# Kernel tuning notes

Hardware: AMD Instinct MI355X
Metric: run time of the kernel (lower is better)

## Reference

```python
import jax, jax.numpy as jnp
import numpy as np
from jax import lax

T_SIZE = 8        # frames
S_SIZE = 14       # spatial grid side
N_HEAD = 16
D_MODEL = 1024
L = S_SIZE * S_SIZE          # 196 patch tokens per frame
N_BATCH = 8


def _layernorm(x, g, b):
    # torch LayerNorm subclass computes in fp32 then casts back
    x32 = x.astype(jnp.float32)
    m = x32.mean(-1, keepdims=True)
    v = x32.var(-1, keepdims=True)
    return ((x32 - m) * lax.rsqrt(v + 1e-5) * g + b).astype(x.dtype)


def _mha(x, wqkv, bqkv, wo, bo, bias):
    # x: [S, B, C] seq-first like torch MHA; bias: [n_head, S, S] or None
    S, B, C = x.shape
    hd = C // N_HEAD
    qkv = x @ wqkv.T + bqkv
    q, k, v = jnp.split(qkv, 3, axis=-1)
    def h(t):
        return t.reshape(S, B, N_HEAD, hd).transpose(1, 2, 0, 3)  # [B,H,S,hd]
    q = h(q) * (1.0 / np.sqrt(hd))
    k, v = h(k), h(v)
    scores = jnp.einsum('bhqd,bhkd->bhqk', q, k)
    if bias is not None:
        scores = scores + bias[None]  # broadcast over batch (torch repeats; same math)
    a = jax.nn.softmax(scores, axis=-1)
    o = jnp.einsum('bhqk,bhkd->bhqd', a, v).transpose(2, 0, 1, 3).reshape(S, B, C)
    return o @ wo.T + bo


def _rel_idx():
    t = jnp.arange(T_SIZE)
    idx_t = t[:, None] - t[None, :] + T_SIZE - 1          # [T,T]
    c = jnp.arange(L)
    qi, qj = c // S_SIZE, c % S_SIZE
    i_off = qi[:, None] - qi[None, :] + S_SIZE - 1
    j_off = qj[:, None] - qj[None, :] + S_SIZE - 1
    idx_s = i_off * (2 * S_SIZE - 1) + j_off              # [L,L]
    return idx_t, idx_s


def reference(x, pos_w, pos_b, ln_t_g, ln_t_b, rpb_t, wqkv_t, bqkv_t, wo_t, bo_t,
              ln1_g, ln1_b, rpb_s, wqkv_s, bqkv_s, wo_s, bo_s,
              ln2_g, ln2_b, fc_w, fc_b, proj_w, proj_b):
    T, S, H, C = T_SIZE, S_SIZE, N_HEAD, D_MODEL
    LT = L * T
    N = x.shape[1]
    idx_t, idx_s = _rel_idx()

    # depthwise 3D conv positional embedding on patch tokens (token order is (h w t))
    v = x[1:].reshape(S, S, T, N, C).transpose(3, 4, 2, 0, 1)  # [N,C,T,H,W]
    conv = lax.conv_general_dilated(
        v, pos_w, (1, 1, 1), [(1, 1), (1, 1), (1, 1)],
        dimension_numbers=('NCDHW', 'OIDHW', 'NCDHW'),
        feature_group_count=C) + pos_b[None, :, None, None, None]
    tmp = (v + conv).reshape(N, C, T, L).transpose(3, 2, 0, 1).reshape(LT, N, C)
    x = jnp.concatenate([x[:1], tmp], 0)

    # temporal attention: '(l t) n c -> t (n l) c'
    xt = x[1:].reshape(L, T, N, C).transpose(1, 2, 0, 3).reshape(T, N * L, C)
    bias_t = rpb_t[idx_t].transpose(2, 0, 1)  # [H,T,T]
    rt = _mha(_layernorm(xt, ln_t_g, ln_t_b), wqkv_t, bqkv_t, wo_t, bo_t, bias_t)
    rt = rt.reshape(T, N, L, C).transpose(2, 0, 1, 3).reshape(LT, N, C)
    xt_full = x[1:] + rt

    # spatial attention with replicated cls token: 'l (t n) c' batching
    cls = jnp.tile(x[:1], (1, T, 1))                      # [1, T*N, C], t-major
    xs = jnp.concatenate([cls, xt_full.reshape(L, T * N, C)], 0)  # [L+1, T*N, C]
    bias_s = jnp.zeros((H, L + 1, L + 1), x.dtype).at[:, 1:, 1:].set(
        rpb_s[idx_s].transpose(2, 0, 1))
    rs = _mha(_layernorm(xs, ln1_g, ln1_b), wqkv_s, bqkv_s, wo_s, bo_s, bias_s)
    cls_out = rs[0].reshape(T, N, C).mean(0, keepdims=True)       # mean over frames
    spa = rs[1:].reshape(LT, N, C)                                # 'l (t n) -> (l t) n'
    x = x + jnp.concatenate([cls_out, spa], 0)

    # MLP with QuickGELU
    h = _layernorm(x, ln2_g, ln2_b) @ fc_w.T + fc_b
    h = h * jax.nn.sigmoid(1.702 * h)
    return x + (h @ proj_w.T + proj_b)


def setup_inputs() -> dict:
    key = jax.random.key(0)
    ks = jax.random.split(key, 12)
    C = D_MODEL
    f32 = jnp.float32
    def w(k, shape, s=0.02):
        return jax.random.normal(k, shape, f32) * s
    return {
        'x': jax.random.normal(ks[0], (1 + L * T_SIZE, N_BATCH, C), f32),
        'pos_w': w(ks[1], (C, 1, 3, 3, 3)),
        'pos_b': jnp.zeros((C,), f32),
        'ln_t_g': jnp.ones((C,), f32), 'ln_t_b': jnp.zeros((C,), f32),
        'rpb_t': w(ks[2], (2 * T_SIZE - 1, N_HEAD)),
        'wqkv_t': w(ks[3], (3 * C, C)), 'bqkv_t': jnp.zeros((3 * C,), f32),
        'wo_t': w(ks[4], (C, C)), 'bo_t': jnp.zeros((C,), f32),
        'ln1_g': jnp.ones((C,), f32), 'ln1_b': jnp.zeros((C,), f32),
        'rpb_s': w(ks[5], ((2 * S_SIZE - 1) ** 2, N_HEAD)),
        'wqkv_s': w(ks[6], (3 * C, C)), 'bqkv_s': jnp.zeros((3 * C,), f32),
        'wo_s': w(ks[7], (C, C)), 'bo_s': jnp.zeros((C,), f32),
        'ln2_g': jnp.ones((C,), f32), 'ln2_b': jnp.zeros((C,), f32),
        'fc_w': w(ks[8], (4 * C, C)), 'fc_b': jnp.zeros((4 * C,), f32),
        'proj_w': w(ks[9], (C, 4 * C)), 'proj_b': jnp.zeros((C,), f32),
    }
```

## Files before the change

### kernel.cpp

```cpp
#include <hip/hip_runtime.h>
#include <stdint.h>

typedef unsigned short u16;
typedef __attribute__((ext_vector_type(8))) __bf16 bf16x8;
typedef __attribute__((ext_vector_type(4))) float f32x4;

__device__ __forceinline__ float bf2f(u16 u) {
    return __uint_as_float(((unsigned int)u) << 16);
}
__device__ __forceinline__ u16 f2bf(float f) {
    unsigned int u = __float_as_uint(f);
    u += 0x7fffu + ((u >> 16) & 1u);
    return (u16)(u >> 16);
}

__device__ __forceinline__ void gl16(const u16* g, u16* l) {
    __builtin_amdgcn_global_load_lds(
        (const __attribute__((address_space(1))) unsigned int*)(uintptr_t)g,
        (__attribute__((address_space(3))) unsigned int*)(uintptr_t)l,
        16, 0, 0);
}

__global__ __launch_bounds__(256) void cvt_bf16(const float4* __restrict__ in,
                                                ushort4* __restrict__ out, int n4) {
    int tid = blockIdx.x * 256 + threadIdx.x;
    if (tid < n4) {
        float4 v = in[tid];
        ushort4 o;
        o.x = f2bf(v.x); o.y = f2bf(v.y); o.z = f2bf(v.z); o.w = f2bf(v.w);
        out[tid] = o;
    }
}

__global__ __launch_bounds__(256) void cvt_wt(const float* __restrict__ pw,
                                              float* __restrict__ wt) {
    int tid = blockIdx.x * 256 + threadIdx.x;
    if (tid < 27648) {
        int tap = tid >> 10, c = tid & 1023;
        wt[tid] = pw[c * 27 + tap];
    }
}

__global__ __launch_bounds__(256) void posembed(const float4* __restrict__ x4,
                                                const float4* __restrict__ wt4,
                                                const float4* __restrict__ pb4,
                                                float4* __restrict__ out4) {
    int tid = blockIdx.x * 256 + threadIdx.x;
    float4 xv = x4[tid];
    int rf = tid >> 11;
    if (rf == 0) { out4[tid] = xv; return; }
    int c4 = tid & 255;
    int n = (tid >> 8) & 7;
    int r = rf - 1;
    int t = r & 7, l = r >> 3;
    int i = l / 14, j = l - i * 14;
    float4 pbv = pb4[c4];
    float a0 = xv.x + pbv.x, a1 = xv.y + pbv.y, a2 = xv.z + pbv.z, a3 = xv.w + pbv.w;
#pragma unroll
    for (int dt = 0; dt < 3; dt++) {
        int tt = t + dt - 1;
        if (tt < 0 || tt > 7) continue;
#pragma unroll
        for (int di = 0; di < 3; di++) {
            int ii = i + di - 1;
            if (ii < 0 || ii > 13) continue;
#pragma unroll
            for (int dj = 0; dj < 3; dj++) {
                int jj = j + dj - 1;
                if (jj < 0 || jj > 13) continue;
                float4 w4 = wt4[(dt * 9 + di * 3 + dj) * 256 + c4];
                float4 v = x4[(size_t)(1 + ((ii * 14 + jj) << 3) + tt) * 2048 + (n << 8) + c4];
                a0 += w4.x * v.x; a1 += w4.y * v.y; a2 += w4.z * v.z; a3 += w4.w * v.w;
            }
        }
    }
    out4[tid] = (float4){a0, a1, a2, a3};
}

__global__ __launch_bounds__(256) void ln_kernel(const float* __restrict__ resid,
                                                 const u16* __restrict__ Radd,
                                                 const float* __restrict__ g,
                                                 const float* __restrict__ bb,
                                                 u16* __restrict__ out, int mode) {
    int ro = blockIdx.x;
    int tid = threadIdx.x;
    int src, n;
    long long rarow = -1;
    if (mode == 0) {
        int t = ro / 1568, b2 = ro - t * 1568;
        n = b2 / 196;
        int l = b2 - n * 196;
        src = 1 + l * 8 + t;
    } else if (mode == 1) {
        int s = ro >> 6, u = ro & 63;
        int t = u >> 3;
        n = u & 7;
        if (s == 0) src = 0;
        else { src = 1 + (s - 1) * 8 + t; rarow = (long long)(t * 1568 + n * 196 + (s - 1)); }
    } else {
        src = ro >> 3;
        n = ro & 7;
    }
    const float* xp = resid + ((size_t)src * 8 + n) * 1024 + tid * 4;
    float4 xv = *(const float4*)xp;
    float x0 = xv.x, x1 = xv.y, x2 = xv.z, x3 = xv.w;
    if (rarow >= 0) {
        const u16* rp = Radd + rarow * 1024 + tid * 4;
        x0 += bf2f(rp[0]); x1 += bf2f(rp[1]); x2 += bf2f(rp[2]); x3 += bf2f(rp[3]);
    }
    float s1 = x0 + x1 + x2 + x3;
    float s2 = x0 * x0 + x1 * x1 + x2 * x2 + x3 * x3;
#pragma unroll
    for (int off = 32; off > 0; off >>= 1) {
        s1 += __shfl_down(s1, off);
        s2 += __shfl_down(s2, off);
    }
    __shared__ float red[8];
    int lane = tid & 63, w = tid >> 6;
    if (lane == 0) { red[w] = s1; red[4 + w] = s2; }
    __syncthreads();
    float S1 = red[0] + red[1] + red[2] + red[3];
    float S2 = red[4] + red[5] + red[6] + red[7];
    float mean = S1 * (1.f / 1024.f);
    float var = S2 * (1.f / 1024.f) - mean * mean;
    float rstd = rsqrtf(var + 1e-5f);
    int c = tid * 4;
    u16* op = out + (size_t)ro * 1024 + c;
    op[0] = f2bf((x0 - mean) * rstd * g[c + 0] + bb[c + 0]);
    op[1] = f2bf((x1 - mean) * rstd * g[c + 1] + bb[c + 1]);
    op[2] = f2bf((x2 - mean) * rstd * g[c + 2] + bb[c + 2]);
    op[3] = f2bf((x3 - mean) * rstd * g[c + 3] + bb[c + 3]);
}

__global__ __launch_bounds__(256) void gemm_bf16(const u16* __restrict__ A,
                                                 const u16* __restrict__ W,
                                                 const float* __restrict__ bias,
                                                 u16* __restrict__ Co,
                                                 int M, int N, int K, int gelu,
                                                 int nx) {
    __shared__ u16 As[2][128 * 32];
    __shared__ u16 Bs[2][128 * 32];
    int tid = threadIdx.x;
    int T = gridDim.x;
    int bid = blockIdx.x;
    int w_ = (bid & 7) * (T >> 3) + (bid >> 3);
    int n0 = (w_ % nx) * 128;
    int m0 = (w_ / nx) * 128;
    int lane = tid & 63, wid = tid >> 6;
    int wm = (wid >> 1) * 64, wn = (wid & 1) * 64;
    int lm = lane & 15, q = lane >> 4;

    f32x4 acc[4][4];
#pragma unroll
    for (int i = 0; i < 4; i++)
#pragma unroll
        for (int j = 0; j < 4; j++) acc[i][j] = (f32x4){0.f, 0.f, 0.f, 0.f};

    int r0 = wid * 32 + (lane >> 2);
    int colb = (lane & 3) * 8;
    int mA0 = m0 + r0;          if (mA0 > M - 1) mA0 = M - 1;
    int mA1 = m0 + r0 + 16;     if (mA1 > M - 1) mA1 = M - 1;
    const u16* gA0 = A + (size_t)mA0 * K + colb;
    const u16* gA1 = A + (size_t)mA1 * K + colb;
    const u16* gB0 = W + (size_t)(n0 + r0) * K + colb;
    const u16* gB1 = W + (size_t)(n0 + r0 + 16) * K + colb;
    int wo = wid * 1024;

    auto loadt = [&](int b) {
        gl16(gA0, &As[b][wo]); gl16(gA1, &As[b][wo + 512]);
        gl16(gB0, &Bs[b][wo]); gl16(gB1, &Bs[b][wo + 512]);
        gA0 += 32; gA1 += 32; gB0 += 32; gB1 += 32;
    };
    auto comput = [&](int b) {
        bf16x8 af[4], bfr[4];
#pragma unroll
        for (int i = 0; i < 4; i++) af[i] = *(const bf16x8*)&As[b][(wm + i * 16 + lm) * 32 + q * 8];
#pragma unroll
        for (int j = 0; j < 4; j++) bfr[j] = *(const bf16x8*)&Bs[b][(wn + j * 16 + lm) * 32 + q * 8];
#pragma unroll
        for (int i = 0; i < 4; i++)
#pragma unroll
            for (int j = 0; j < 4; j++)
                acc[i][j] = __builtin_amdgcn_mfma_f32_16x16x32_bf16(af[i], bfr[j], acc[i][j], 0, 0, 0);
    };

    int Tt = K >> 5;
    loadt(0);
    __syncthreads();
    loadt(1); comput(0); __syncthreads();
    for (int t = 2; t + 1 < Tt; t += 2) {
        loadt(0); comput(1); __syncthreads();
        loadt(1); comput(0); __syncthreads();
    }
    comput(1);

#pragma unroll
    for (int i = 0; i < 4; i++) {
        int row_b = m0 + wm + i * 16 + q * 4;
#pragma unroll
        for (int j = 0; j < 4; j++) {
            int col = n0 + wn + j * 16 + lm;
            float bv = bias[col];
#pragma unroll
            for (int r = 0; r < 4; r++) {
                int row = row_b + r;
                if (row < M) {
                    float v = acc[i][j][r] + bv;
                    if (gelu) v = v / (1.f + __expf(-1.702f * v));
                    Co[(size_t)row * N + col] = f2bf(v);
                }
            }
        }
    }
}

__global__ __launch_bounds__(512) void gemm256(const u16* __restrict__ A,
                                               const u16* __restrict__ W,
                                               const float* __restrict__ bias,
                                               u16* __restrict__ Co,
                                               float* __restrict__ Fout,
                                               int M, int N, int K, int gelu,
                                               int nnt) {
    __shared__ __align__(16) u16 sA[2][16384];
    __shared__ __align__(16) u16 sB[2][16384];
    int tid = threadIdx.x;
    int wid = tid >> 6, lane = tid & 63;
    int wr = wid >> 2, wc = wid & 3;
    int lm = lane & 15, q = lane >> 4;

    int nwg = gridDim.x, orig = blockIdx.x;
    int qq = nwg >> 3, rr = nwg & 7, xcd = orig & 7, blk = orig >> 3;
    int wg = (xcd < rr ? xcd * (qq + 1) : rr * (qq + 1) + (xcd - rr) * qq) + blk;
    int n0 = (wg % nnt) * 256, m0 = (wg / nnt) * 256;

    int NT = K >> 6, NTm1 = NT - 1;

    int rl = wid * 8 + (lane >> 3);
    int cl = ((lane & 7) ^ (rl & 7)) * 8;
    const u16* pA[4];
    const u16* pB[4];
#pragma unroll
    for (int h2 = 0; h2 < 4; h2++) {
        int ra = m0 + h2 * 64 + rl; if (ra > M - 1) ra = M - 1;
        int rb = n0 + h2 * 64 + rl; if (rb > N - 1) rb = N - 1;
        pA[h2] = A + (size_t)ra * K + cl;
        pB[h2] = W + (size_t)rb * K + cl;
    }
    int ldst = wid * 512;

    f32x4 acc[8][4];
#pragma unroll
    for (int i = 0; i < 8; i++)
#pragma unroll
        for (int j = 0; j < 4; j++) acc[i][j] = (f32x4){0.f, 0.f, 0.f, 0.f};

    bf16x8 af[4][2];
    bf16x8 bfv[4][2];

#define STG(P, D, b, h, kt) do { \
        int _k = (kt); if (_k > NTm1) _k = NTm1; \
        gl16(P[(h) * 2] + (size_t)_k * 64, &D[b][(h) * 8192 + ldst]); \
        gl16(P[(h) * 2 + 1] + (size_t)_k * 64, &D[b][(h) * 8192 + 4096 + ldst]); \
    } while (0)
#define LDA_(b, ih) do { \
        _Pragma("unroll") for (int iq = 0; iq < 4; iq++) \
        _Pragma("unroll") for (int kk = 0; kk < 2; kk++) \
            af[iq][kk] = *(const bf16x8*)&sA[b][((ih) * 128 + wr * 64 + iq * 16 + lm) * 64 + \
                                                (((q + kk * 4) ^ (lm & 7)) * 8)]; \
    } while (0)
#define LDB_(b, jh) do { \
        _Pragma("unroll") for (int jq = 0; jq < 2; jq++) \
        _Pragma("unroll") for (int kk = 0; kk < 2; kk++) \
            bfv[(jh) * 2 + jq][kk] = *(const bf16x8*)&sB[b][((jh) * 128 + wc * 32 + jq * 16 + lm) * 64 + \
                                                            (((q + kk * 4) ^ (lm & 7)) * 8)]; \
    } while (0)
#define MMA_(ih, jh) do { \
        __builtin_amdgcn_s_setprio(1); \
        _Pragma("unroll") for (int iq = 0; iq < 4; iq++) \
        _Pragma("unroll") for (int jq = 0; jq < 2; jq++) \
        _Pragma("unroll") for (int kk = 0; kk < 2; kk++) \
            acc[(ih) * 4 + iq][(jh) * 2 + jq] = __builtin_amdgcn_mfma_f32_16x16x32_bf16( \
                af[iq][kk], bfv[(jh) * 2 + jq][kk], acc[(ih) * 4 + iq][(jh) * 2 + jq], 0, 0, 0); \
        __builtin_amdgcn_s_setprio(0); \
    } while (0)
#define BAR asm volatile("s_barrier" ::: "memory")
#define VM6 asm volatile("s_waitcnt vmcnt(6)" ::: "memory")

    STG(pA, sA, 0, 0, 0);
    STG(pA, sA, 0, 1, 0);
    STG(pB, sB, 0, 0, 0);
    STG(pB, sB, 0, 1, 0);
    STG(pA, sA, 1, 0, 1);
    STG(pB, sB, 1, 1, 1);
    STG(pA, sA, 1, 1, 1);
    VM6;
    BAR;

    int S = NT >> 1;
    for (int s = 0; s < S; s++) {
        int t = s * 2;
        LDA_(0, 0); LDB_(0, 0);
        STG(pB, sB, 1, 0, t + 1);
        BAR; MMA_(0, 0); BAR;
        LDB_(0, 1);
        STG(pA, sA, 0, 0, t + 2);
        BAR; MMA_(0, 1); BAR;
        LDA_(0, 1);
        STG(pB, sB, 0, 1, t + 2);
        BAR; MMA_(1, 1); BAR;
        STG(pA, sA, 0, 1, t + 2);
        VM6;
        BAR; MMA_(1, 0); BAR;
        LDA_(1, 0); LDB_(1, 0);
        STG(pB, sB, 0, 0, t + 2);
        BAR; MMA_(0, 0); BAR;
        LDB_(1, 1);
        STG(pA, sA, 1, 0, t + 3);
        BAR; MMA_(0, 1); BAR;
        LDA_(1, 1);
        STG(pB, sB, 1, 1, t + 3);
        BAR; MMA_(1, 1); BAR;
        STG(pA, sA, 1, 1, t + 3);
        VM6;
        BAR; MMA_(1, 0); BAR;
    }
    asm volatile("s_waitcnt vmcnt(0)" ::: "memory");

#pragma unroll
    for (int ih = 0; ih < 2; ih++)
#pragma unroll
        for (int iq = 0; iq < 4; iq++) {
            int row_b = m0 + ih * 128 + wr * 64 + iq * 16 + q * 4;
#pragma unroll
            for (int jh = 0; jh < 2; jh++)
#pragma unroll
                for (int jq = 0; jq < 2; jq++) {
                    int col = n0 + jh * 128 + wc * 32 + jq * 16 + lm;
                    float bv = bias[col];
#pragma unroll
                    for (int r = 0; r < 4; r++) {
                        int row = row_b + r;
                        if (row < M) {
                            float v = acc[ih * 4 + iq][jh * 2 + jq][r] + bv;
                            if (gelu) v = v / (1.f + __expf(-1.702f * v));
                            if (Fout) {
                                size_t o = (size_t)row * N + col;
                                Fout[o] = Fout[o] + v;
                            } else {
                                Co[(size_t)row * N + col] = f2bf(v);
                            }
                        }
                    }
                }
        }
#undef STG
#undef LDA_
#undef LDB_
#undef MMA_
#undef BAR
#undef VM6
}

__global__ __launch_bounds__(64) void attn_t(const u16* __restrict__ qkv,
                                             const float* __restrict__ rpb,
                                             u16* __restrict__ out) {
    int blk = blockIdx.x;
    int b = blk % 1568, h = blk / 1568;
    int d = threadIdx.x;
    __shared__ float qs[8][65], ks[8][65], vs[8][65];
    __shared__ float ps[8][9];
#pragma unroll
    for (int t = 0; t < 8; t++) {
        size_t row = (size_t)(t * 1568 + b) * 3072 + h * 64 + d;
        qs[t][d] = bf2f(qkv[row]) * 0.125f;
        ks[t][d] = bf2f(qkv[row + 1024]);
        vs[t][d] = bf2f(qkv[row + 2048]);
    }
    __syncthreads();
    int tq = d >> 3, tk = d & 7;
    float s = rpb[(tq - tk + 7) * 16 + h];
#pragma unroll
    for (int dd = 0; dd < 64; dd++) s += qs[tq][dd] * ks[tk][dd];
    float mx = s;
    mx = fmaxf(mx, __shfl_xor(mx, 1));
    mx = fmaxf(mx, __shfl_xor(mx, 2));
    mx = fmaxf(mx, __shfl_xor(mx, 4));
    float p = __expf(s - mx);
    float su = p;
    su += __shfl_xor(su, 1);
    su += __shfl_xor(su, 2);
    su += __shfl_xor(su, 4);
    ps[tq][tk] = p / su;
    __syncthreads();
#pragma unroll
    for (int t2 = 0; t2 < 8; t2++) {
        float o = 0.f;
#pragma unroll
        for (int k2 = 0; k2 < 8; k2++) o += ps[t2][k2] * vs[k2][d];
        out[(size_t)(t2 * 1568 + b) * 1024 + h * 64 + d] = f2bf(o);
    }
}

#define KLS 72
#define PVS 232
__global__ __launch_bounds__(256) void attn_s(const u16* __restrict__ qkv,
                                              const float* __restrict__ rpb,
                                              u16* __restrict__ out) {
    __shared__ u16 Kl[208 * KLS];
    __shared__ u16 Vt[64 * PVS];
    __shared__ u16 Pl[4][16 * PVS];
    __shared__ float rpb_l[736];
    int blk = blockIdx.x;
    int u = blk & 63, h = blk >> 6;
    int tid = threadIdx.x;
    int w = tid >> 6, lane = tid & 63;
    int lm = lane & 15, quad = lane >> 4;

    for (int idx = tid; idx < 197 * 8; idx += 256) {
        int s = idx >> 3, c8 = idx & 7;
        const u16* gp = qkv + (size_t)(s * 64 + u) * 3072 + h * 64 + c8 * 8;
        uint4 kv = *(const uint4*)(gp + 1024);
        uint4 vv = *(const uint4*)(gp + 2048);
        *(uint4*)&Kl[s * KLS + c8 * 8] = kv;
        const u16* vp = (const u16*)&vv;
#pragma unroll
        for (int j = 0; j < 8; j++) Vt[(c8 * 8 + j) * PVS + s] = vp[j];
    }
    for (int i = tid; i < 11 * KLS; i += 256) Kl[197 * KLS + i] = 0;
    for (int i = tid; i < 64 * 35; i += 256) {
        int dd = i / 35, c = 197 + (i - dd * 35);
        Vt[dd * PVS + c] = 0;
    }
    {
        for (int i = lane; i < 256; i += 64) {
            int r = i >> 4, c = 208 + (i & 15);
            Pl[w][r * PVS + c] = 0;
        }
    }
    for (int i = tid; i < 729; i += 256) rpb_l[i] = rpb[i * 16 + h];
    __syncthreads();

    for (int it = 0; it < 4; it++) {
        int qt = it * 4 + w;
        bool act = qt < 13;
        f32x4 sc[13];
        float rs[4];
        if (act) {
            int qrow = qt * 16 + lm;
            int srq = qrow > 196 ? 196 : qrow;
            const u16* qp = qkv + (size_t)(srq * 64 + u) * 3072 + h * 64 + quad * 8;
            bf16x8 aq0 = *(const bf16x8*)qp;
            bf16x8 aq1 = *(const bf16x8*)(qp + 32);
            for (int kt = 0; kt < 13; kt++) {
                bf16x8 bk0 = *(const bf16x8*)&Kl[(kt * 16 + lm) * KLS + quad * 8];
                bf16x8 bk1 = *(const bf16x8*)&Kl[(kt * 16 + lm) * KLS + 32 + quad * 8];
                f32x4 s = __builtin_amdgcn_mfma_f32_16x16x32_bf16(aq0, bk0, (f32x4){0.f, 0.f, 0.f, 0.f}, 0, 0, 0);
                sc[kt] = __builtin_amdgcn_mfma_f32_16x16x32_bf16(aq1, bk1, s, 0, 0, 0);
            }
            int tk = lm;
#pragma unroll
            for (int r = 0; r < 4; r++) {
                int qr = qt * 16 + quad * 4 + r;
                int qcl = qr > 196 ? 196 : qr;
                int lq = qcl - 1;
                int qi = lq / 14, qj = lq - qi * 14;
                for (int kt = 0; kt < 13; kt++) {
                    int tkk = kt * 16 + tk;
                    float v;
                    if (tkk >= 197) v = -1e30f;
                    else {
                        v = sc[kt][r] * 0.125f;
                        if (qr >= 1 && tkk >= 1) {
                            int lk = tkk - 1;
                            int ki = lk / 14, kj = lk - ki * 14;
                            v += rpb_l[(qi - ki + 13) * 27 + (qj - kj + 13)];
                        }
                    }
                    sc[kt][r] = v;
                }
                float mx = -3e38f;
                for (int kt = 0; kt < 13; kt++) mx = fmaxf(mx, sc[kt][r]);
                mx = fmaxf(mx, __shfl_xor(mx, 1));
                mx = fmaxf(mx, __shfl_xor(mx, 2));
                mx = fmaxf(mx, __shfl_xor(mx, 4));
                mx = fmaxf(mx, __shfl_xor(mx, 8));
                float sm = 0.f;
                for (int kt = 0; kt < 13; kt++) {
                    float p = __expf(sc[kt][r] - mx);
                    sc[kt][r] = p;
                    sm += p;
                }
                sm += __shfl_xor(sm, 1);
                sm += __shfl_xor(sm, 2);
                sm += __shfl_xor(sm, 4);
                sm += __shfl_xor(sm, 8);
                rs[r] = sm;
                for (int kt = 0; kt < 13; kt++)
                    Pl[w][(quad * 4 + r) * PVS + kt * 16 + tk] = f2bf(sc[kt][r]);
            }
        }
        __syncthreads();
        if (act) {
            bf16x8 pa[7];
#pragma unroll
            for (int kc = 0; kc < 7; kc++)
                pa[kc] = *(const bf16x8*)&Pl[w][lm * PVS + kc * 32 + quad * 8];
#pragma unroll
            for (int ct = 0; ct < 4; ct++) {
                f32x4 o = (f32x4){0.f, 0.f, 0.f, 0.f};
#pragma unroll
                for (int kc = 0; kc < 7; kc++) {
                    bf16x8 vb = *(const bf16x8*)&Vt[(ct * 16 + lm) * PVS + kc * 32 + quad * 8];
                    o = __builtin_amdgcn_mfma_f32_16x16x32_bf16(pa[kc], vb, o, 0, 0, 0);
                }
#pragma unroll
                for (int r = 0; r < 4; r++) {
                    int qr = qt * 16 + quad * 4 + r;
                    if (qr < 197)
                        out[(size_t)(qr * 64 + u) * 1024 + h * 64 + ct * 16 + lm] =
                            f2bf(o[r] / rs[r]);
                }
            }
        }
        __syncthreads();
    }
}

__global__ __launch_bounds__(256) void add_cls(const u16* __restrict__ R, float4* __restrict__ resid4) {
    int tid = blockIdx.x * 256 + threadIdx.x;
    int c4 = tid & 255, n = tid >> 8;
    float s0 = 0.f, s1 = 0.f, s2 = 0.f, s3 = 0.f;
#pragma unroll
    for (int t = 0; t < 8; t++) {
        ushort4 rv = *(const ushort4*)&R[(size_t)(t * 8 + n) * 1024 + c4 * 4];
        s0 += bf2f(rv.x); s1 += bf2f(rv.y); s2 += bf2f(rv.z); s3 += bf2f(rv.w);
    }
    float4 v = resid4[tid];
    v.x += s0 * 0.125f; v.y += s1 * 0.125f; v.z += s2 * 0.125f; v.w += s3 * 0.125f;
    resid4[tid] = v;
}

__global__ __launch_bounds__(256) void add_spa(const u16* __restrict__ R, float4* __restrict__ resid4) {
    int tid = blockIdx.x * 256 + threadIdx.x;
    int c4 = tid & 255;
    int n = (tid >> 8) & 7;
    int r = tid >> 11;
    int t = r & 7, l = r >> 3;
    int srow = (l + 1) * 64 + t * 8 + n;
    ushort4 rv = *(const ushort4*)&R[(size_t)srow * 1024 + c4 * 4];
    float4 v = resid4[tid + 2048];
    v.x += bf2f(rv.x); v.y += bf2f(rv.y); v.z += bf2f(rv.z); v.w += bf2f(rv.w);
    resid4[tid + 2048] = v;
}

extern "C" void kernel_launch(void* const* d_in, const int* in_sizes, int n_in,
                              void* d_out, int out_size, void* d_ws, size_t ws_size,
                              hipStream_t stream) {
    const float* x      = (const float*)d_in[0];
    const float* pos_w  = (const float*)d_in[1];
    const float* pos_b  = (const float*)d_in[2];
    const float* ln_t_g = (const float*)d_in[3];
    const float* ln_t_b = (const float*)d_in[4];
    const float* rpb_t  = (const float*)d_in[5];
    const float* wqkv_t = (const float*)d_in[6];
    const float* bqkv_t = (const float*)d_in[7];
    const float* wo_t   = (const float*)d_in[8];
    const float* bo_t   = (const float*)d_in[9];
    const float* ln1_g  = (const float*)d_in[10];
    const float* ln1_b  = (const float*)d_in[11];
    const float* rpb_s  = (const float*)d_in[12];
    const float* wqkv_s = (const float*)d_in[13];
    const float* bqkv_s = (const float*)d_in[14];
    const float* wo_s   = (const float*)d_in[15];
    const float* bo_s   = (const float*)d_in[16];
    const float* ln2_g  = (const float*)d_in[17];
    const float* ln2_b  = (const float*)d_in[18];
    const float* fc_w   = (const float*)d_in[19];
    const float* fc_b   = (const float*)d_in[20];
    const float* proj_w = (const float*)d_in[21];
    const float* proj_b = (const float*)d_in[22];
    float* resid = (float*)d_out;

    u16* Wq_t  = (u16*)d_ws;
    u16* Wo_t  = Wq_t + 3145728;
    u16* Wq_s  = Wo_t + 1048576;
    u16* Wo_s  = Wq_s + 3145728;
    u16* Wfc   = Wo_s + 1048576;
    u16* Wpj   = Wfc  + 4194304;
    u16* Albuf = Wpj  + 4194304;
    u16* QKV   = Albuf + 12910592;
    u16* Obuf  = QKV   + 38731776;
    u16* Rbuf  = Obuf  + 12910592;
    u16* Hbuf  = QKV;
    float* wt  = (float*)QKV;

    cvt_bf16<<<3072, 256, 0, stream>>>((const float4*)wqkv_t, (ushort4*)Wq_t, 786432);
    cvt_bf16<<<1024, 256, 0, stream>>>((const float4*)wo_t,   (ushort4*)Wo_t, 262144);
    cvt_bf16<<<3072, 256, 0, stream>>>((const float4*)wqkv_s, (ushort4*)Wq_s, 786432);
    cvt_bf16<<<1024, 256, 0, stream>>>((const float4*)wo_s,   (ushort4*)Wo_s, 262144);
    cvt_bf16<<<4096, 256, 0, stream>>>((const float4*)fc_w,   (ushort4*)Wfc,  1048576);
    cvt_bf16<<<4096, 256, 0, stream>>>((const float4*)proj_w, (ushort4*)Wpj,  1048576);
    cvt_wt<<<108, 256, 0, stream>>>(pos_w, wt);

    posembed<<<12552, 256, 0, stream>>>((const float4*)x, (const float4*)wt,
                                        (const float4*)pos_b, (float4*)resid);

    ln_kernel<<<12544, 256, 0, stream>>>(resid, nullptr, ln_t_g, ln_t_b, Albuf, 0);
    gemm_bf16<<<2352, 256, 0, stream>>>(Albuf, Wq_t, bqkv_t, QKV, 12544, 3072, 1024, 0, 24);
    attn_t<<<25088, 64, 0, stream>>>(QKV, rpb_t, Obuf);
    gemm_bf16<<<784, 256, 0, stream>>>(Obuf, Wo_t, bo_t, Rbuf, 12544, 1024, 1024, 0, 8);

    ln_kernel<<<12608, 256, 0, stream>>>(resid, Rbuf, ln1_g, ln1_b, Albuf, 1);
    gemm_bf16<<<2376, 256, 0, stream>>>(Albuf, Wq_s, bqkv_s, QKV, 12608, 3072, 1024, 0, 24);
    attn_s<<<1024, 256, 0, stream>>>(QKV, rpb_s, Obuf);
    gemm_bf16<<<792, 256, 0, stream>>>(Obuf, Wo_s, bo_s, Rbuf, 12608, 1024, 1024, 0, 8);
    add_cls<<<8, 256, 0, stream>>>(Rbuf, (float4*)resid);
    add_spa<<<12544, 256, 0, stream>>>(Rbuf, (float4*)resid);

    ln_kernel<<<12552, 256, 0, stream>>>(resid, nullptr, ln2_g, ln2_b, Albuf, 2);
    gemm_bf16<<<3168, 256, 0, stream>>>(Albuf, Wfc, fc_b, Hbuf, 12552, 4096, 1024, 1, 32);
    gemm256<<<200, 512, 0, stream>>>(Hbuf, Wpj, proj_b, nullptr, resid,
                                     12552, 1024, 4096, 0, 4);
}
```

Baseline: 1.152 ms.

## Fuse spatial residual add into out-proj GEMM, merge weight casts, vectorize loads

The separate weight-conversion launches become one multi-segment kernel. The spatial-attention output projection now adds its result straight into the fp32 residual for patch rows and writes bf16 only for the cls rows, which removes the add_spa kernel and its bf16 round trip. LayerNorm gamma/beta and the temporal-attention QKV loads are vectorized, and the shared-memory padding changes. The fused epilogue does scattered fp32 read-modify-write stores, and it skips the bf16 rounding of R for spatial rows, which slightly changes numerics.

```diff
diff --git a/kernel.cpp b/kernel.cpp
--- a/kernel.cpp
+++ b/kernel.cpp
@@ -21,15 +21,25 @@
         16, 0, 0);
 }
 
-__global__ __launch_bounds__(256) void cvt_bf16(const float4* __restrict__ in,
-                                                ushort4* __restrict__ out, int n4) {
-    int tid = blockIdx.x * 256 + threadIdx.x;
-    if (tid < n4) {
-        float4 v = in[tid];
-        ushort4 o;
-        o.x = f2bf(v.x); o.y = f2bf(v.y); o.z = f2bf(v.z); o.w = f2bf(v.w);
-        out[tid] = o;
-    }
+__global__ __launch_bounds__(256) void cvt_all(const float4* __restrict__ a0, ushort4* __restrict__ o0,
+                                               const float4* __restrict__ a1, ushort4* __restrict__ o1,
+                                               const float4* __restrict__ a2, ushort4* __restrict__ o2,
+                                               const float4* __restrict__ a3, ushort4* __restrict__ o3,
+                                               const float4* __restrict__ a4, ushort4* __restrict__ o4,
+                                               const float4* __restrict__ a5, ushort4* __restrict__ o5) {
+    int b = blockIdx.x;
+    const float4* src; ushort4* dst; int base;
+    if      (b < 3072)  { src = a0; dst = o0; base = 0; }
+    else if (b < 4096)  { src = a1; dst = o1; base = 3072; }
+    else if (b < 7168)  { src = a2; dst = o2; base = 4096; }
+    else if (b < 8192)  { src = a3; dst = o3; base = 7168; }
+    else if (b < 12288) { src = a4; dst = o4; base = 8192; }
+    else                { src = a5; dst = o5; base = 12288; }
+    int tid = (b - base) * 256 + threadIdx.x;
+    float4 v = src[tid];
+    ushort4 o;
+    o.x = f2bf(v.x); o.y = f2bf(v.y); o.z = f2bf(v.z); o.w = f2bf(v.w);
+    dst[tid] = o;
 }
 
 __global__ __launch_bounds__(256) void cvt_wt(const float* __restrict__ pw,
@@ -125,11 +135,13 @@
     float var = S2 * (1.f / 1024.f) - mean * mean;
     float rstd = rsqrtf(var + 1e-5f);
     int c = tid * 4;
+    float4 gv = *(const float4*)(g + c);
+    float4 bv = *(const float4*)(bb + c);
     u16* op = out + (size_t)ro * 1024 + c;
-    op[0] = f2bf((x0 - mean) * rstd * g[c + 0] + bb[c + 0]);
-    op[1] = f2bf((x1 - mean) * rstd * g[c + 1] + bb[c + 1]);
-    op[2] = f2bf((x2 - mean) * rstd * g[c + 2] + bb[c + 2]);
-    op[3] = f2bf((x3 - mean) * rstd * g[c + 3] + bb[c + 3]);
+    op[0] = f2bf((x0 - mean) * rstd * gv.x + bv.x);
+    op[1] = f2bf((x1 - mean) * rstd * gv.y + bv.y);
+    op[2] = f2bf((x2 - mean) * rstd * gv.z + bv.z);
+    op[3] = f2bf((x3 - mean) * rstd * gv.w + bv.w);
 }
 
 __global__ __launch_bounds__(256) void gemm_bf16(const u16* __restrict__ A,
@@ -208,6 +220,95 @@
                     float v = acc[i][j][r] + bv;
                     if (gelu) v = v / (1.f + __expf(-1.702f * v));
                     Co[(size_t)row * N + col] = f2bf(v);
+                }
+            }
+        }
+    }
+}
+
+__global__ __launch_bounds__(256) void gemm_wos(const u16* __restrict__ A,
+                                                const u16* __restrict__ W,
+                                                const float* __restrict__ bias,
+                                                u16* __restrict__ Rb,
+                                                float* __restrict__ resid,
+                                                int M, int nx) {
+    const int N = 1024, K = 1024;
+    __shared__ u16 As[2][128 * 32];
+    __shared__ u16 Bs[2][128 * 32];
+    int tid = threadIdx.x;
+    int T = gridDim.x;
+    int bid = blockIdx.x;
+    int w_ = (bid & 7) * (T >> 3) + (bid >> 3);
+    int n0 = (w_ % nx) * 128;
+    int m0 = (w_ / nx) * 128;
+    int lane = tid & 63, wid = tid >> 6;
+    int wm = (wid >> 1) * 64, wn = (wid & 1) * 64;
+    int lm = lane & 15, q = lane >> 4;
+
+    f32x4 acc[4][4];
+#pragma unroll
+    for (int i = 0; i < 4; i++)
+#pragma unroll
+        for (int j = 0; j < 4; j++) acc[i][j] = (f32x4){0.f, 0.f, 0.f, 0.f};
+
+    int r0 = wid * 32 + (lane >> 2);
+    int colb = (lane & 3) * 8;
+    int mA0 = m0 + r0;          if (mA0 > M - 1) mA0 = M - 1;
+    int mA1 = m0 + r0 + 16;     if (mA1 > M - 1) mA1 = M - 1;
+    const u16* gA0 = A + (size_t)mA0 * K + colb;
+    const u16* gA1 = A + (size_t)mA1 * K + colb;
+    const u16* gB0 = W + (size_t)(n0 + r0) * K + colb;
+    const u16* gB1 = W + (size_t)(n0 + r0 + 16) * K + colb;
+    int wo = wid * 1024;
+
+    auto loadt = [&](int b) {
+        gl16(gA0, &As[b][wo]); gl16(gA1, &As[b][wo + 512]);
+        gl16(gB0, &Bs[b][wo]); gl16(gB1, &Bs[b][wo + 512]);
+        gA0 += 32; gA1 += 32; gB0 += 32; gB1 += 32;
+    };
+    auto comput = [&](int b) {
+        bf16x8 af[4], bfr[4];
+#pragma unroll
+        for (int i = 0; i < 4; i++) af[i] = *(const bf16x8*)&As[b][(wm + i * 16 + lm) * 32 + q * 8];
+#pragma unroll
+        for (int j = 0; j < 4; j++) bfr[j] = *(const bf16x8*)&Bs[b][(wn + j * 16 + lm) * 32 + q * 8];
+#pragma unroll
+        for (int i = 0; i < 4; i++)
+#pragma unroll
+            for (int j = 0; j < 4; j++)
+                acc[i][j] = __builtin_amdgcn_mfma_f32_16x16x32_bf16(af[i], bfr[j], acc[i][j], 0, 0, 0);
+    };
+
+    int Tt = K >> 5;
+    loadt(0);
+    __syncthreads();
+    loadt(1); comput(0); __syncthreads();
+    for (int t = 2; t + 1 < Tt; t += 2) {
+        loadt(0); comput(1); __syncthreads();
+        loadt(1); comput(0); __syncthreads();
+    }
+    comput(1);
+
+#pragma unroll
+    for (int i = 0; i < 4; i++) {
+        int row_b = m0 + wm + i * 16 + q * 4;
+#pragma unroll
+        for (int j = 0; j < 4; j++) {
+            int col = n0 + wn + j * 16 + lm;
+            float bv = bias[col];
+#pragma unroll
+            for (int r = 0; r < 4; r++) {
+                int row = row_b + r;
+                if (row < M) {
+                    float v = acc[i][j][r] + bv;
+                    if (row < 64) {
+                        Rb[(size_t)row * N + col] = f2bf(v);
+                    } else {
+                        int s = row >> 6, u = row & 63;
+                        int t2 = u >> 3, n = u & 7;
+                        size_t o = ((size_t)(1 + (s - 1) * 8 + t2) * 8 + n) * 1024 + col;
+                        resid[o] = resid[o] + v;
+                    }
                 }
             }
         }
@@ -367,14 +468,22 @@
     int blk = blockIdx.x;
     int b = blk % 1568, h = blk / 1568;
     int d = threadIdx.x;
-    __shared__ float qs[8][65], ks[8][65], vs[8][65];
+    __shared__ float qs[8][68], ks[8][68], vs[8][68];
     __shared__ float ps[8][9];
 #pragma unroll
-    for (int t = 0; t < 8; t++) {
-        size_t row = (size_t)(t * 1568 + b) * 3072 + h * 64 + d;
-        qs[t][d] = bf2f(qkv[row]) * 0.125f;
-        ks[t][d] = bf2f(qkv[row + 1024]);
-        vs[t][d] = bf2f(qkv[row + 2048]);
+    for (int tt = 0; tt < 2; tt++) {
+        int t = tt * 4 + (d >> 4);
+        int c4 = (d & 15) * 4;
+        size_t row = (size_t)(t * 1568 + b) * 3072 + h * 64 + c4;
+        ushort4 qv = *(const ushort4*)(qkv + row);
+        ushort4 kv = *(const ushort4*)(qkv + row + 1024);
+        ushort4 vv = *(const ushort4*)(qkv + row + 2048);
+        qs[t][c4 + 0] = bf2f(qv.x) * 0.125f; qs[t][c4 + 1] = bf2f(qv.y) * 0.125f;
+        qs[t][c4 + 2] = bf2f(qv.z) * 0.125f; qs[t][c4 + 3] = bf2f(qv.w) * 0.125f;
+        ks[t][c4 + 0] = bf2f(kv.x); ks[t][c4 + 1] = bf2f(kv.y);
+        ks[t][c4 + 2] = bf2f(kv.z); ks[t][c4 + 3] = bf2f(kv.w);
+        vs[t][c4 + 0] = bf2f(vv.x); vs[t][c4 + 1] = bf2f(vv.y);
+        vs[t][c4 + 2] = bf2f(vv.z); vs[t][c4 + 3] = bf2f(vv.w);
     }
     __syncthreads();
     int tq = d >> 3, tk = d & 7;
@@ -540,19 +649,6 @@
     resid4[tid] = v;
 }
 
-__global__ __launch_bounds__(256) void add_spa(const u16* __restrict__ R, float4* __restrict__ resid4) {
-    int tid = blockIdx.x * 256 + threadIdx.x;
-    int c4 = tid & 255;
-    int n = (tid >> 8) & 7;
-    int r = tid >> 11;
-    int t = r & 7, l = r >> 3;
-    int srow = (l + 1) * 64 + t * 8 + n;
-    ushort4 rv = *(const ushort4*)&R[(size_t)srow * 1024 + c4 * 4];
-    float4 v = resid4[tid + 2048];
-    v.x += bf2f(rv.x); v.y += bf2f(rv.y); v.z += bf2f(rv.z); v.w += bf2f(rv.w);
-    resid4[tid + 2048] = v;
-}
-
 extern "C" void kernel_launch(void* const* d_in, const int* in_sizes, int n_in,
                               void* d_out, int out_size, void* d_ws, size_t ws_size,
                               hipStream_t stream) {
@@ -594,12 +690,13 @@
     u16* Hbuf  = QKV;
     float* wt  = (float*)QKV;
 
-    cvt_bf16<<<3072, 256, 0, stream>>>((const float4*)wqkv_t, (ushort4*)Wq_t, 786432);
-    cvt_bf16<<<1024, 256, 0, stream>>>((const float4*)wo_t,   (ushort4*)Wo_t, 262144);
-    cvt_bf16<<<3072, 256, 0, stream>>>((const float4*)wqkv_s, (ushort4*)Wq_s, 786432);
-    cvt_bf16<<<1024, 256, 0, stream>>>((const float4*)wo_s,   (ushort4*)Wo_s, 262144);
-    cvt_bf16<<<4096, 256, 0, stream>>>((const float4*)fc_w,   (ushort4*)Wfc,  1048576);
-    cvt_bf16<<<4096, 256, 0, stream>>>((const float4*)proj_w, (ushort4*)Wpj,  1048576);
+    cvt_all<<<16384, 256, 0, stream>>>(
+        (const float4*)wqkv_t, (ushort4*)Wq_t,
+        (const float4*)wo_t,   (ushort4*)Wo_t,
+        (const float4*)wqkv_s, (ushort4*)Wq_s,
+        (const float4*)wo_s,   (ushort4*)Wo_s,
+        (const float4*)fc_w,   (ushort4*)Wfc,
+        (const float4*)proj_w, (ushort4*)Wpj);
     cvt_wt<<<108, 256, 0, stream>>>(pos_w, wt);
 
     posembed<<<12552, 256, 0, stream>>>((const float4*)x, (const float4*)wt,
@@ -613,9 +710,8 @@
     ln_kernel<<<12608, 256, 0, stream>>>(resid, Rbuf, ln1_g, ln1_b, Albuf, 1);
     gemm_bf16<<<2376, 256, 0, stream>>>(Albuf, Wq_s, bqkv_s, QKV, 12608, 3072, 1024, 0, 24);
     attn_s<<<1024, 256, 0, stream>>>(QKV, rpb_s, Obuf);
-    gemm_bf16<<<792, 256, 0, stream>>>(Obuf, Wo_s, bo_s, Rbuf, 12608, 1024, 1024, 0, 8);
+    gemm_wos<<<792, 256, 0, stream>>>(Obuf, Wo_s, bo_s, Rbuf, resid, 12608, 8);
     add_cls<<<8, 256, 0, stream>>>(Rbuf, (float4*)resid);
-    add_spa<<<12544, 256, 0, stream>>>(Rbuf, (float4*)resid);
 
     ln_kernel<<<12552, 256, 0, stream>>>(resid, nullptr, ln2_g, ln2_b, Albuf, 2);
     gemm_bf16<<<3168, 256, 0, stream>>>(Albuf, Wfc, fc_b, Hbuf, 12552, 4096, 1024, 1, 32);
```

Result: faster. 1.110 ms (-3.7%).
